# Kernel optimization log

Measured on AMD Instinct MI355X. Metric: run time of the kernel, lower is better.

Reference implementation:

```python
import jax, jax.numpy as jnp
import numpy as np

H, D = 8, 8            # heads, per-head dim (hid_dim = 64)
HID = H * D
L = 6                  # HGTConv layers
NI, NV = 32768, 131072 # num 'instr' / 'var' nodes (batch_size == NI)
E_VV, E_VI, E_IV = 1048576, 524288, 524288
INV_SQRT_D = float(1.0 / np.sqrt(D))


def _seg_softmax(logits, seg, n):
    # softmax over edges grouped by destination node (PyG softmax semantics)
    m = jax.ops.segment_max(logits, seg, num_segments=n)
    m = jnp.where(jnp.isfinite(m), m, 0.0)
    e = jnp.exp(logits - m[seg])
    s = jax.ops.segment_sum(e, seg, num_segments=n)
    return e / (s[seg] + 1e-16)


def _edge_msg(k_src, v_src, q_dst, arel, mrel, prel, src, dst, n_dst):
    # relation-specific transforms: [N_src,H,D] x [H,D,D] -> [N_src,H,D]
    k_rel = jnp.einsum('nhd,hde->nhe', k_src, arel)
    v_rel = jnp.einsum('nhd,hde->nhe', v_src, mrel)
    alpha = jnp.einsum('ehd,ehd->eh', q_dst[dst], k_rel[src]) * prel * INV_SQRT_D  # [E,H]
    w = _seg_softmax(alpha, dst, n_dst)
    return jax.ops.segment_sum(v_rel[src] * w[:, :, None], dst, num_segments=n_dst)


def _kqv(x, Wk, Wq, Wv, bk, bq, bv, n):
    k = (x @ Wk.T + bk).reshape(n, H, D)
    q = (x @ Wq.T + bq).reshape(n, H, D)
    v = (x @ Wv.T + bv).reshape(n, H, D)
    return k, q, v


def _forward(x_instr, x_var,
             Wk_i, Wq_i, Wv_i, Wa_i, bk_i, bq_i, bv_i, ba_i, skip_i,
             Wk_v, Wq_v, Wv_v, Wa_v, bk_v, bq_v, bv_v, ba_v, skip_v,
             arel_vv, mrel_vv, prel_vv, arel_vi, mrel_vi, prel_vi,
             arel_iv, mrel_iv, prel_iv,
             Wqkv, bqkv, Wo, bo,
             mw0, mb0, mw1, mb1, mw2, mb2, mw3, mb3, mw4, mb4, mw5, mb5,
             src_vv, dst_vv, src_vi, dst_vi, src_iv, dst_iv):
    xi, xv = x_instr, x_var
    outs = []
    for l in range(L):
        k_i, q_i, v_i = _kqv(xi, Wk_i[l], Wq_i[l], Wv_i[l], bk_i[l], bq_i[l], bv_i[l], NI)
        k_v, q_v, v_v = _kqv(xv, Wk_v[l], Wq_v[l], Wv_v[l], bk_v[l], bq_v[l], bv_v[l], NV)
        # per-edge-type attention softmax + scatter-sum, then sum over edge types (group='sum')
        agg_v = (_edge_msg(k_v, v_v, q_v, arel_vv[l], mrel_vv[l], prel_vv[l], src_vv, dst_vv, NV)
                 + _edge_msg(k_i, v_i, q_v, arel_iv[l], mrel_iv[l], prel_iv[l], src_iv, dst_iv, NV))
        agg_i = _edge_msg(k_v, v_v, q_i, arel_vi[l], mrel_vi[l], prel_vi[l], src_vi, dst_vi, NI)
        o_i = jax.nn.gelu(agg_i.reshape(NI, HID), approximate=False) @ Wa_i[l].T + ba_i[l]
        b_i = jax.nn.sigmoid(skip_i[l])
        xi = b_i * o_i + (1.0 - b_i) * xi
        o_v = jax.nn.gelu(agg_v.reshape(NV, HID), approximate=False) @ Wa_v[l].T + ba_v[l]
        b_v = jax.nn.sigmoid(skip_v[l])
        xv = b_v * o_v + (1.0 - b_v) * xv
        if l > 0:
            outs.append(xi)
    # jumping-knowledge MultiheadAttention over the L-1 stacked layer outputs
    x = jnp.stack(outs)                        # [S, NI, HID], S = L-1 = 5
    S = x.shape[0]
    qkv = x @ Wqkv.T + bqkv                    # [S, NI, 3*HID]
    q, k, v = jnp.split(qkv, 3, axis=-1)
    q = q.reshape(S, NI, H, D)
    k = k.reshape(S, NI, H, D)
    v = v.reshape(S, NI, H, D)
    sc = jnp.einsum('snhd,tnhd->nhst', q, k) * INV_SQRT_D
    w = jax.nn.softmax(sc, axis=-1)
    o = jnp.einsum('nhst,tnhd->snhd', w, v).reshape(S, NI, HID)
    o = o @ Wo.T + bo
    out = o.sum(axis=0)                        # [NI, HID]; batch_size == NI so view is identity
    for W, b in ((mw0, mb0), (mw1, mb1), (mw2, mb2), (mw3, mb3), (mw4, mb4)):
        out = jax.nn.gelu(out @ W.T + b, approximate=False)
    out = out @ mw5.T + mb5                    # [NI, 1]
    return out[:, 0]


def setup_inputs() -> dict:
    key = jax.random.key(0)
    ks = iter(jax.random.split(key, 64))
    def nrm(shape, scale=1.0):
        return jax.random.normal(next(ks), shape, dtype=jnp.float32) * scale
    d = {}
    d['x_instr'] = nrm((NI, HID))
    d['x_var'] = nrm((NV, HID))
    for t in ('i', 'v'):
        for p in ('Wk', 'Wq', 'Wv', 'Wa'):
            d[f'{p}_{t}'] = nrm((L, HID, HID), (2.0 / HID) ** 0.5)
        for p in ('bk', 'bq', 'bv', 'ba'):
            d[f'{p}_{t}'] = jnp.zeros((L, HID), jnp.float32)
        d[f'skip_{t}'] = jnp.ones((L,), jnp.float32)
    for e in ('vv', 'vi', 'iv'):
        d[f'arel_{e}'] = nrm((L, H, D, D), (1.0 / D) ** 0.5)
        d[f'mrel_{e}'] = nrm((L, H, D, D), (1.0 / D) ** 0.5)
        d[f'prel_{e}'] = jnp.ones((L, H), jnp.float32)
    d['Wqkv'] = nrm((3 * HID, HID), (2.0 / HID) ** 0.5)
    d['bqkv'] = jnp.zeros((3 * HID,), jnp.float32)
    d['Wo'] = nrm((HID, HID), (2.0 / HID) ** 0.5)
    d['bo'] = jnp.zeros((HID,), jnp.float32)
    dims = [64, 32, 16, 8, 4, 2, 1]
    for i in range(6):
        d[f'mw{i}'] = nrm((dims[i + 1], dims[i]), (2.0 / dims[i]) ** 0.5)
        d[f'mb{i}'] = jnp.zeros((dims[i + 1],), jnp.float32)
    d['src_vv'] = jax.random.randint(next(ks), (E_VV,), 0, NV, dtype=jnp.int32).astype(jnp.int64)
    d['dst_vv'] = jax.random.randint(next(ks), (E_VV,), 0, NV, dtype=jnp.int32).astype(jnp.int64)
    d['src_vi'] = jax.random.randint(next(ks), (E_VI,), 0, NV, dtype=jnp.int32).astype(jnp.int64)
    d['dst_vi'] = jax.random.randint(next(ks), (E_VI,), 0, NI, dtype=jnp.int32).astype(jnp.int64)
    d['src_iv'] = jax.random.randint(next(ks), (E_IV,), 0, NI, dtype=jnp.int32).astype(jnp.int64)
    d['dst_iv'] = jax.random.randint(next(ks), (E_IV,), 0, NV, dtype=jnp.int32).astype(jnp.int64)
    return d


def reference(x_instr, x_var,
              Wk_i, Wq_i, Wv_i, Wa_i, bk_i, bq_i, bv_i, ba_i, skip_i,
              Wk_v, Wq_v, Wv_v, Wa_v, bk_v, bq_v, bv_v, ba_v, skip_v,
              arel_vv, mrel_vv, prel_vv, arel_vi, mrel_vi, prel_vi,
              arel_iv, mrel_iv, prel_iv,
              Wqkv, bqkv, Wo, bo,
              mw0, mb0, mw1, mb1, mw2, mb2, mw3, mb3, mw4, mb4, mw5, mb5,
              src_vv, dst_vv, src_vi, dst_vi, src_iv, dst_iv):
    return _forward(x_instr, x_var,
                    Wk_i, Wq_i, Wv_i, Wa_i, bk_i, bq_i, bv_i, ba_i, skip_i,
                    Wk_v, Wq_v, Wv_v, Wa_v, bk_v, bq_v, bv_v, ba_v, skip_v,
                    arel_vv, mrel_vv, prel_vv, arel_vi, mrel_vi, prel_vi,
                    arel_iv, mrel_iv, prel_iv,
                    Wqkv, bqkv, Wo, bo,
                    mw0, mb0, mw1, mb1, mw2, mb2, mw3, mb3, mw4, mb4, mw5, mb5,
                    src_vv, dst_vv, src_vi, dst_vi, src_iv, dst_iv)
```

## Files before the change

### kernel.cpp

```cpp
#include <hip/hip_runtime.h>
#include <cmath>

typedef _Float16 f16_t;
typedef __attribute__((ext_vector_type(8))) short short8;
typedef __attribute__((ext_vector_type(8))) _Float16 half8;
typedef __attribute__((ext_vector_type(4))) float f32x4;
typedef _Float16 h2v __attribute__((ext_vector_type(2)));
typedef _Float16 h8 __attribute__((ext_vector_type(8)));

#define NI_N 32768
#define NV_N 131072
#define E_VV 1048576
#define E_VI 524288
#define E_IV 524288
#define NT_N (NV_N+NV_N+NI_N)
#define ET_N (E_VV+E_IV+E_VI)
#define SC_WIN 4
#define LOG2E 1.4426950408889634f
#define CHV 192
#define CHI 64
#define CHQ 256

__device__ __forceinline__ float gelu_f(float x){ return 0.5f*x*(1.0f+erff(x*0.7071067811865476f)); }

__device__ __forceinline__ void splitf16(float v, short& hi, short& lo){
  f16_t h=(f16_t)v;
  hi=__builtin_bit_cast(short,h);
  f16_t l=(f16_t)(v-(float)h);
  lo=__builtin_bit_cast(short,l);
}
__device__ __forceinline__ f32x4 mfma16(short8 a, short8 b, f32x4 c){
  return __builtin_amdgcn_mfma_f32_16x16x32_f16(__builtin_bit_cast(half8,a),__builtin_bit_cast(half8,b),c,0,0,0);
}
__device__ __forceinline__ float fexp2(float x){
#if __has_builtin(__builtin_amdgcn_exp2f)
  return __builtin_amdgcn_exp2f(x);
#else
  return exp2f(x);
#endif
}
__device__ __forceinline__ float ldval(const float* p){ return *p; }
__device__ __forceinline__ float ldval(const f16_t* p){ return (float)*p; }
__device__ __forceinline__ void stval(float* p,float v){ *p=v; }
__device__ __forceinline__ void stval(f16_t* p,float v){ *p=(f16_t)v; }
__device__ __forceinline__ h2v shxor(h2v a,int m){
  return __builtin_bit_cast(h2v,__shfl_xor(__builtin_bit_cast(int,a),m));
}

__global__ __launch_bounds__(256) void k_hist3(const int* __restrict__ dvv,const int* __restrict__ div_,
    const int* __restrict__ dvi,int* __restrict__ cnt){
  int i=blockIdx.x*256+threadIdx.x;
  if(i<E_VV) atomicAdd(&cnt[dvv[i]],1);
  else if(i<E_VV+E_IV) atomicAdd(&cnt[NV_N+div_[i-E_VV]],1);
  else atomicAdd(&cnt[2*NV_N+dvi[i-E_VV-E_IV]],1);
}
__global__ __launch_bounds__(512) void k_scan1(const int* __restrict__ cnt,int N,int* __restrict__ rp,int* __restrict__ bsum){
  __shared__ int sh[512];
  int i=blockIdx.x*512+threadIdx.x;
  int v=(i<N)?cnt[i]:0;
  sh[threadIdx.x]=v; __syncthreads();
  for(int off=1;off<512;off<<=1){
    int t=(threadIdx.x>=(unsigned)off)?sh[threadIdx.x-off]:0; __syncthreads();
    sh[threadIdx.x]+=t; __syncthreads();
  }
  if(i<N) rp[i]=sh[threadIdx.x]-v;
  if(threadIdx.x==511) bsum[blockIdx.x]=sh[511];
}
__global__ __launch_bounds__(1024) void k_scan2(const int* __restrict__ bsum,int* __restrict__ boff,int nb){
  __shared__ int sh[1024];
  int t=threadIdx.x;
  int v=(t<nb)?bsum[t]:0;
  sh[t]=v; __syncthreads();
  for(int off=1;off<1024;off<<=1){
    int x=(t>=(unsigned)off)?sh[t-off]:0; __syncthreads();
    sh[t]+=x; __syncthreads();
  }
  if(t<nb) boff[t]=sh[t]-v;
  if(t==1023) boff[nb]=sh[1023];
}
__global__ __launch_bounds__(512) void k_scan3(int* __restrict__ rp,const int* __restrict__ boff,int* __restrict__ cur,int N,int nb){
  int i=blockIdx.x*512+threadIdx.x;
  if(i<N){ int v=rp[i]+boff[i>>9]; rp[i]=v; cur[i]=v; }
  if(i==0) rp[N]=boff[nb];
}
__global__ __launch_bounds__(256) void k_scatter3w(const int* __restrict__ svv,const int* __restrict__ dvv,
    const int* __restrict__ siv,const int* __restrict__ div_,
    const int* __restrict__ svi,const int* __restrict__ dvi,
    int* __restrict__ cur,int* __restrict__ esrc,int dlo,int dhi){
  int i=blockIdx.x*256+threadIdx.x;
  int d,s;
  if(i<E_VV){ d=dvv[i]; if(d<dlo||d>=dhi) return; s=svv[i]*320; }
  else if(i<E_VV+E_IV){ int j=i-E_VV; d=NV_N+div_[j]; if(d<dlo||d>=dhi) return; s=siv[j]*192; }
  else { int j=i-E_VV-E_IV; d=2*NV_N+dvi[j]; if(d<dlo||d>=dhi) return; s=svi[j]*320; }
  int p=atomicAdd(&cur[d],1); esrc[p]=s;
}

__global__ __launch_bounds__(256) void k_castx(const float* __restrict__ xi_in,const float* __restrict__ xv_in,
    f16_t* __restrict__ xi,f16_t* __restrict__ xv){
  int i=blockIdx.x*256+threadIdx.x;
  if(i<NI_N*64) xi[i]=(f16_t)xi_in[i];
  else { int j=i-NI_N*64; xv[j]=(f16_t)xv_in[j]; }
}

struct FoldArgs{
  const float *Wk_i,*Wq_i,*Wv_i,*bk_i,*bq_i,*bv_i;
  const float *Wk_v,*Wq_v,*Wv_v,*bk_v,*bq_v,*bv_v;
  const float *arel_vv,*mrel_vv,*prel_vv,*arel_vi,*mrel_vi,*prel_vi,*arel_iv,*mrel_iv,*prel_iv;
  const float *Wa_i,*Wa_v;
  short *fwh_var,*fwl_var,*fwh_ins,*fwl_ins,*wah_i,*wal_i,*wah_v,*wal_v;
  float *fwb_var,*fwb_ins;
};
__global__ __launch_bounds__(256) void k_fold6(FoldArgs fa){
  int gid=blockIdx.x*256+threadIdx.x;
  if(gid>=6*640*64) return;
  int l=gid/(640*64);
  int rem=gid-l*640*64;
  int r=rem>>6, c=rem&63;
  if(r>=512){
    int ro=r&63;
    const float* W=(r<576)?fa.Wa_i:fa.Wa_v;
    short *sh=((r<576)?fa.wah_i:fa.wah_v)+l*4096, *sl=((r<576)?fa.wal_i:fa.wal_v)+l*4096;
    short h,lo; splitf16(W[l*4096+ro*64+c],h,lo);
    sh[ro*64+c]=h; sl[ro*64+c]=lo;
    return;
  }
  const float *W,*B,*rel=nullptr,*prl=nullptr;
  short *sh,*sl; float *fwb; int orow,d; bool isq=false;
  if(r<320){
    sh=fa.fwh_var+l*320*64; sl=fa.fwl_var+l*320*64; fwb=fa.fwb_var+l*320;
    d=r&63;
    if(r<64){ W=fa.Wq_v; B=fa.bq_v; orow=d; isq=true; }
    else if(r<128){ W=fa.Wk_v; B=fa.bk_v; rel=fa.arel_vv; prl=fa.prel_vv; orow=64+2*d; }
    else if(r<192){ W=fa.Wv_v; B=fa.bv_v; rel=fa.mrel_vv; orow=64+2*d+1; }
    else if(r<256){ W=fa.Wk_v; B=fa.bk_v; rel=fa.arel_vi; prl=fa.prel_vi; orow=192+2*d; }
    else         { W=fa.Wv_v; B=fa.bv_v; rel=fa.mrel_vi; orow=192+2*d+1; }
  }else{
    int rr=r-320; sh=fa.fwh_ins+l*192*64; sl=fa.fwl_ins+l*192*64; fwb=fa.fwb_ins+l*192;
    d=rr&63;
    if(rr<64){ W=fa.Wq_i; B=fa.bq_i; orow=d; isq=true; }
    else if(rr<128){ W=fa.Wk_i; B=fa.bk_i; rel=fa.arel_iv; prl=fa.prel_iv; orow=64+2*d; }
    else           { W=fa.Wv_i; B=fa.bv_i; rel=fa.mrel_iv; orow=64+2*d+1; }
  }
  float val,bval;
  if(!rel){
    val=W[l*4096+d*64+c]; bval=B[l*64+d];
  }else{
    int h=d>>3, e=d&7;
    float s=prl?prl[l*8+h]*0.3535533905932738f:1.0f;
    float acc=0.f,bacc=0.f;
    #pragma unroll
    for(int dd=0;dd<8;dd++){
      float rv=rel[l*512+h*64+dd*8+e];
      acc += W[l*4096+(h*8+dd)*64+c]*rv;
      bacc+= B[l*64+h*8+dd]*rv;
    }
    val=acc*s; bval=bacc*s;
  }
  if(isq){ val*=LOG2E; bval*=LOG2E; }
  short h2q,lo2; splitf16(val,h2q,lo2);
  sh[orow*64+c]=h2q; sl[orow*64+c]=lo2;
  if(c==0) fwb[orow]=bval;
}

__global__ __launch_bounds__(256) void k_split2(const float* __restrict__ W,int n,short* __restrict__ hi,short* __restrict__ lo){
  int i=blockIdx.x*256+threadIdx.x;
  if(i<n){ short h,l2; splitf16(W[i],h,l2); hi[i]=h; lo[i]=l2; }
}

__device__ __forceinline__ void colres_body(const f16_t* __restrict__ A,int nrb,
    const short* __restrict__ Bh,const short* __restrict__ Bl,
    const float* __restrict__ bias,f16_t* __restrict__ out,int octot,int ocol0,
    int c,int CH,int wave,int lane,int m,int quad,f16_t (*rep)[72])
{
  short8 bhi[4][2], blo[4][2]; float bb[4];
  #pragma unroll
  for(int ot=0;ot<4;ot++){
    size_t o=(size_t)(ocol0+ot*16+m)*64+quad*8;
    bhi[ot][0]=*(const short8*)(Bh+o);    bhi[ot][1]=*(const short8*)(Bh+o+32);
    blo[ot][0]=*(const short8*)(Bl+o);    blo[ot][1]=*(const short8*)(Bl+o+32);
    bb[ot]=bias[ocol0+ot*16+m];
  }
  int rr0=lane>>3, seg=lane&7;
  for(int rb=c;rb<nrb;rb+=CH){
    int row0=rb*64+wave*16;
    const f16_t* ap=A+(size_t)(row0+m)*64+quad*8;
    short8 a0=*(const short8*)(const void*)ap;
    short8 a1=*(const short8*)(const void*)(ap+32);
    f32x4 acc[4];
    #pragma unroll
    for(int ot=0;ot<4;ot++){ f32x4 t={bb[ot],bb[ot],bb[ot],bb[ot]}; acc[ot]=t; }
    #pragma unroll
    for(int ot=0;ot<4;ot++){
      acc[ot]=mfma16(a0,blo[ot][0],acc[ot]);
      acc[ot]=mfma16(a0,bhi[ot][0],acc[ot]);
      acc[ot]=mfma16(a1,blo[ot][1],acc[ot]);
      acc[ot]=mfma16(a1,bhi[ot][1],acc[ot]);
    }
    #pragma unroll
    for(int ot=0;ot<4;ot++)
      #pragma unroll
      for(int r=0;r<4;r++)
        rep[quad*4+r][ot*16+m]=(f16_t)acc[ot][r];
    #pragma unroll
    for(int it=0;it<2;it++){
      int rr=it*8+rr0;
      h8 vals=*(const h8*)&rep[rr][seg*8];
      *(h8*)(out+(size_t)(row0+rr)*octot+ocol0+seg*8)=vals;
    }
  }
}

__global__ __launch_bounds__(256) void k_colres_feat(const f16_t* __restrict__ Av,const f16_t* __restrict__ Ai,
    const short* __restrict__ Bvh,const short* __restrict__ Bvl,const float* __restrict__ biasv,
    const short* __restrict__ Bih,const short* __restrict__ Bil,const float* __restrict__ biasi,
    f16_t* __restrict__ outv,f16_t* __restrict__ outi)
{
  __shared__ f16_t rep[4][16][72];
  const int wave=threadIdx.x>>6, lane=threadIdx.x&63;
  const int m=lane&15, quad=lane>>4;
  int bx=blockIdx.x;
  if(bx<5*CHV){
    int pan=bx/CHV, c=bx%CHV;
    colres_body(Av,NV_N/64,Bvh,Bvl,biasv,outv,320,pan*64,c,CHV,wave,lane,m,quad,rep[wave]);
  }else{
    bx-=5*CHV;
    int pan=bx/CHI, c=bx%CHI;
    colres_body(Ai,NI_N/64,Bih,Bil,biasi,outi,192,pan*64,c,CHI,wave,lane,m,quad,rep[wave]);
  }
}

__global__ __launch_bounds__(256) void k_colres1(const f16_t* __restrict__ A,int nrb,
    const short* __restrict__ Bh,const short* __restrict__ Bl,
    const float* __restrict__ bias,f16_t* __restrict__ out,int octot,int CH)
{
  __shared__ f16_t rep[4][16][72];
  const int wave=threadIdx.x>>6, lane=threadIdx.x&63;
  const int m=lane&15, quad=lane>>4;
  int pan=blockIdx.x/CH, c=blockIdx.x%CH;
  colres_body(A,nrb,Bh,Bl,bias,out,octot,pan*64,c,CH,wave,lane,m,quad,rep[wave]);
}

template<typename AT, typename OT>
__device__ __forceinline__ void gemm_body(const AT* __restrict__ A,int row0,
    const short* __restrict__ Bh,const short* __restrict__ Bl,
    const float* __restrict__ bias,float bias_scale,
    OT* __restrict__ out,int octot,int ocol0,int npanels,int m,int quad,int lane,
    f16_t (*rep)[72])
{
  const AT* ap=A+(size_t)(row0+m)*64+quad*8;
  constexpr bool AF16 = (sizeof(AT)==2);
  short8 ahi[2], alo[2];
  if constexpr(AF16){
    #pragma unroll
    for(int kf=0;kf<2;kf++) ahi[kf]=*(const short8*)(const void*)(ap+kf*32);
  }else{
    #pragma unroll
    for(int kf=0;kf<2;kf++){
      short8 th,tl;
      #pragma unroll
      for(int j=0;j<8;j++){ short h,l2; splitf16(ldval(&ap[kf*32+j]),h,l2); th[j]=h; tl[j]=l2; }
      ahi[kf]=th; alo[kf]=tl;
    }
  }
  for(int pan=0;pan<npanels;pan++){
    int colbase=pan*64;
    short8 bhi[4][2], blo[4][2];
    #pragma unroll
    for(int ot=0;ot<4;ot++){
      size_t o=(size_t)(colbase+ot*16+m)*64+quad*8;
      #pragma unroll
      for(int kf=0;kf<2;kf++){
        bhi[ot][kf]=*(const short8*)(Bh+o+kf*32);
        blo[ot][kf]=*(const short8*)(Bl+o+kf*32);
      }
    }
    f32x4 acc[4];
    #pragma unroll
    for(int ot=0;ot<4;ot++){
      float bv=bias[colbase+ot*16+m]*bias_scale;
      acc[ot][0]=bv; acc[ot][1]=bv; acc[ot][2]=bv; acc[ot][3]=bv;
    }
    #pragma unroll
    for(int ot=0;ot<4;ot++){
      #pragma unroll
      for(int kf=0;kf<2;kf++){
        if constexpr(!AF16) acc[ot]=mfma16(alo[kf],bhi[ot][kf],acc[ot]);
        acc[ot]=mfma16(ahi[kf],blo[ot][kf],acc[ot]);
        acc[ot]=mfma16(ahi[kf],bhi[ot][kf],acc[ot]);
      }
    }
    if constexpr(sizeof(OT)==2){
      #pragma unroll
      for(int ot=0;ot<4;ot++)
        #pragma unroll
        for(int r=0;r<4;r++)
          rep[quad*4+r][ot*16+m]=(f16_t)acc[ot][r];
      #pragma unroll
      for(int it=0;it<2;it++){
        int rr=it*8+(lane>>3), seg=lane&7;
        h8 vals=*(const h8*)&rep[rr][seg*8];
        *(h8*)(out+(size_t)(row0+rr)*octot+ocol0+colbase+seg*8)=vals;
      }
    }else{
      #pragma unroll
      for(int ot=0;ot<4;ot++){
        int col=ocol0+colbase+ot*16+m;
        #pragma unroll
        for(int r=0;r<4;r++){
          int row=row0+quad*4+r;
          stval(&out[(size_t)row*octot+col],acc[ot][r]);
        }
      }
    }
  }
}

template<typename AT, typename OT>
__global__ __launch_bounds__(256) void k_gemm64p(const AT* __restrict__ A,int N,
    const short* __restrict__ Bh,const short* __restrict__ Bl,
    const float* __restrict__ bias,float bias_scale,
    OT* __restrict__ out,int octot,int ocol0,int npanels)
{
  __shared__ f16_t rep[4][16][72];
  const int wave=threadIdx.x>>6, lane=threadIdx.x&63;
  const int m=lane&15, quad=lane>>4;
  const int row0=blockIdx.x*64+wave*16;
  if(row0>=N) return;
  gemm_body<AT,OT>(A,row0,Bh,Bl,bias,bias_scale,out,octot,ocol0,npanels,m,quad,lane,rep[wave]);
}

__global__ __launch_bounds__(256) void k_update2(const f16_t* __restrict__ agg_i,const f16_t* __restrict__ agg_v,
    const short* __restrict__ wah_i,const short* __restrict__ wal_i,
    const short* __restrict__ wah_v,const short* __restrict__ wal_v,
    const float* __restrict__ ba_i,const float* __restrict__ ba_v,
    const float* __restrict__ skip_i,const float* __restrict__ skip_v,
    f16_t* __restrict__ x_i,f16_t* __restrict__ x_v,
    f16_t* __restrict__ outs,int nbi)
{
  __shared__ f16_t rep[4][16][72];
  const int wave=threadIdx.x>>6, lane=threadIdx.x&63;
  const int m=lane&15, quad=lane>>4;
  const bool isI=(int)blockIdx.x<nbi;
  const int row0=(isI?blockIdx.x:(blockIdx.x-nbi))*64+wave*16;
  const f16_t* agg=isI?agg_i:agg_v;
  const short* Wah=isI?wah_i:wah_v;
  const short* Wal=isI?wal_i:wal_v;
  const float* ba=isI?ba_i:ba_v;
  const float* skip=isI?skip_i:skip_v;
  f16_t* x=isI?x_i:x_v;
  f16_t* oo=isI?outs:nullptr;
  f16_t (*R)[72]=rep[wave];
  short8 bhi[4][2], blo[4][2];
  #pragma unroll
  for(int ot=0;ot<4;ot++){
    size_t o=(size_t)(ot*16+m)*64+quad*8;
    #pragma unroll
    for(int kf=0;kf<2;kf++){
      bhi[ot][kf]=*(const short8*)(Wah+o+kf*32);
      blo[ot][kf]=*(const short8*)(Wal+o+kf*32);
    }
  }
  const f16_t* ap=agg+(size_t)(row0+m)*64+quad*8;
  short8 ahi[2], alo[2];
  #pragma unroll
  for(int kf=0;kf<2;kf++){
    short8 th,tl;
    #pragma unroll
    for(int j=0;j<8;j++){ short h,l2; splitf16(gelu_f((float)ap[kf*32+j]),h,l2); th[j]=h; tl[j]=l2; }
    ahi[kf]=th; alo[kf]=tl;
  }
  int rr0=lane>>3, seg=lane&7;
  h8 x0=*(const h8*)(x+(size_t)(row0+rr0)*64+seg*8);
  h8 x1=*(const h8*)(x+(size_t)(row0+8+rr0)*64+seg*8);
  *(h8*)&R[rr0][seg*8]=x0;
  *(h8*)&R[8+rr0][seg*8]=x1;
  f32x4 acc[4];
  #pragma unroll
  for(int ot=0;ot<4;ot++){
    float bv=ba[ot*16+m];
    acc[ot][0]=bv; acc[ot][1]=bv; acc[ot][2]=bv; acc[ot][3]=bv;
  }
  #pragma unroll
  for(int ot=0;ot<4;ot++){
    #pragma unroll
    for(int kf=0;kf<2;kf++){
      acc[ot]=mfma16(alo[kf],bhi[ot][kf],acc[ot]);
      acc[ot]=mfma16(ahi[kf],blo[ot][kf],acc[ot]);
      acc[ot]=mfma16(ahi[kf],bhi[ot][kf],acc[ot]);
    }
  }
  float s=1.0f/(1.0f+__expf(-skip[0]));
  #pragma unroll
  for(int ot=0;ot<4;ot++){
    int col=ot*16+m;
    #pragma unroll
    for(int r=0;r<4;r++){
      int row=quad*4+r;
      float xn=s*acc[ot][r]+(1.0f-s)*(float)R[row][col];
      R[row][col]=(f16_t)xn;
    }
  }
  h8 o0=*(const h8*)&R[rr0][seg*8];
  h8 o1=*(const h8*)&R[8+rr0][seg*8];
  *(h8*)(x+(size_t)(row0+rr0)*64+seg*8)=o0;
  *(h8*)(x+(size_t)(row0+8+rr0)*64+seg*8)=o1;
  if(oo){
    *(h8*)(oo+(size_t)(row0+rr0)*64+seg*8)=o0;
    *(h8*)(oo+(size_t)(row0+8+rr0)*64+seg*8)=o1;
  }
}

__device__ __forceinline__ float edge_agg8(const int* __restrict__ rp,const int* __restrict__ es,
    const f16_t* __restrict__ sf,int koff,int n,int lane,f16_t qh)
{
  int b=__builtin_amdgcn_readfirstlane(rp[n]);
  int e=__builtin_amdgcn_readfirstlane(rp[n+1]);
  if(b==e) return 0.f;
  float m=-INFINITY, ls=0.f, acc=0.f;
  h2v q2={qh,qh};
  const int lo2=koff+2*lane;
  for(int i=b;i<e;i+=8){
    int o[8];
    #pragma unroll
    for(int j=0;j<8;j++){
      int idx=i+j; idx=(idx<e)?idx:(e-1);
      o[j]=__builtin_amdgcn_readfirstlane(es[idx]);
    }
    h2v kv[8];
    #pragma unroll
    for(int j=0;j<8;j++) kv[j]=*(const h2v*)(sf+(size_t)(unsigned)o[j]+lo2);
    float p[8];
    #pragma unroll
    for(int jp=0;jp<4;jp++){
      h2v pa={kv[2*jp][0],kv[2*jp+1][0]};
      pa=q2*pa;
      pa=pa+shxor(pa,1);
      pa=pa+shxor(pa,2);
      pa=pa+shxor(pa,4);
      p[2*jp]=(float)pa[0]; p[2*jp+1]=(float)pa[1];
    }
    #pragma unroll
    for(int j=0;j<8;j++) p[j]=(i+j<e)?p[j]:-INFINITY;
    float t0=fmaxf(p[0],p[1]),t1=fmaxf(p[2],p[3]),t2=fmaxf(p[4],p[5]),t3=fmaxf(p[6],p[7]);
    float mn=fmaxf(fmaxf(fmaxf(t0,t1),fmaxf(t2,t3)),m);
    float sc=fexp2(m-mn);
    float w[8];
    #pragma unroll
    for(int j=0;j<8;j++) w[j]=fexp2(p[j]-mn);
    float sw=((w[0]+w[1])+(w[2]+w[3]))+((w[4]+w[5])+(w[6]+w[7]));
    float sa=w[0]*(float)kv[0][1]; sa=fmaf(w[1],(float)kv[1][1],sa);
    float sb=w[2]*(float)kv[2][1]; sb=fmaf(w[3],(float)kv[3][1],sb);
    float sg=w[4]*(float)kv[4][1]; sg=fmaf(w[5],(float)kv[5][1],sg);
    float sd=w[6]*(float)kv[6][1]; sd=fmaf(w[7],(float)kv[7][1],sd);
    ls=fmaf(ls,sc,sw);
    acc=fmaf(acc,sc,(sa+sb)+(sg+sd));
    m=mn;
  }
  return acc/(ls+1e-16f);
}

__global__ __launch_bounds__(256) void k_edge_all(const int* __restrict__ rp_all,const int* __restrict__ es,
    const f16_t* __restrict__ var_feat,const f16_t* __restrict__ ins_feat,
    f16_t* __restrict__ agg_v,f16_t* __restrict__ agg_i,int nbv)
{
  int wave=threadIdx.x>>6, lane=threadIdx.x&63;
  if((int)blockIdx.x<nbv){
    int n=blockIdx.x*4+wave;
    f16_t qh=var_feat[(size_t)n*320+lane];
    float r1=edge_agg8(rp_all,es,var_feat,64,n,lane,qh);
    float r2=edge_agg8(rp_all+NV_N,es,ins_feat,64,n,lane,qh);
    agg_v[(size_t)n*64+lane]=(f16_t)(r1+r2);
  }else{
    int n=(blockIdx.x-nbv)*4+wave;
    f16_t qh=ins_feat[(size_t)n*192+lane];
    float r=edge_agg8(rp_all+2*NV_N,es,var_feat,192,n,lane,qh);
    agg_i[(size_t)n*64+lane]=(f16_t)r;
  }
}

__global__ __launch_bounds__(256) void k_jk(const f16_t* __restrict__ qkv,float* __restrict__ osum,int n_nodes){
  int wave=threadIdx.x>>6, lane=threadIdx.x&63;
  int n=blockIdx.x*4+wave;
  if(n>=n_nodes) return;
  float q[5],k[5],v[5];
  #pragma unroll
  for(int s=0;s<5;s++){
    const f16_t* p=qkv+((size_t)s*n_nodes+n)*192;
    q[s]=(float)p[lane]; k[s]=(float)p[64+lane]; v[s]=(float)p[128+lane];
  }
  float sc[5][5];
  #pragma unroll
  for(int s=0;s<5;s++)
    #pragma unroll
    for(int t=0;t<5;t++){
      float x=q[s]*k[t];
      x+=__shfl_xor(x,1); x+=__shfl_xor(x,2); x+=__shfl_xor(x,4);
      sc[s][t]=x*0.3535533905932738f;
    }
  float os=0.f;
  #pragma unroll
  for(int s=0;s<5;s++){
    float m=sc[s][0];
    #pragma unroll
    for(int t=1;t<5;t++) m=fmaxf(m,sc[s][t]);
    float den=0.f, acc=0.f;
    #pragma unroll
    for(int t=0;t<5;t++){ float e=__expf(sc[s][t]-m); den+=e; acc+=e*v[t]; }
    os+=acc/den;
  }
  osum[(size_t)n*64+lane]=os;
}

struct MlpArgs{ const float *w0,*b0,*w1,*b1,*w2,*b2,*w3,*b3,*w4,*b4,*w5,*b5; };
__global__ __launch_bounds__(256) void k_mlp(const float* __restrict__ in,MlpArgs ma,float* __restrict__ out,int N){
  __shared__ float sw0[2048],sb0[32],sw1[512],sb1[16],sw2[128],sb2[8],sw3[32],sb3[4],sw4[8],sb4[2],sw5[2],sb5[1];
  for(int i=threadIdx.x;i<2048;i+=256) sw0[i]=ma.w0[i];
  for(int i=threadIdx.x;i<512;i+=256)  sw1[i]=ma.w1[i];
  if(threadIdx.x<128) sw2[threadIdx.x]=ma.w2[threadIdx.x];
  if(threadIdx.x<32){ sb0[threadIdx.x]=ma.b0[threadIdx.x]; sw3[threadIdx.x]=ma.w3[threadIdx.x]; }
  if(threadIdx.x<16) sb1[threadIdx.x]=ma.b1[threadIdx.x];
  if(threadIdx.x<8){ sb2[threadIdx.x]=ma.b2[threadIdx.x]; sw4[threadIdx.x]=ma.w4[threadIdx.x]; }
  if(threadIdx.x<4) sb3[threadIdx.x]=ma.b3[threadIdx.x];
  if(threadIdx.x<2){ sb4[threadIdx.x]=ma.b4[threadIdx.x]; sw5[threadIdx.x]=ma.w5[threadIdx.x]; }
  if(threadIdx.x==0) sb5[0]=ma.b5[0];
  __syncthreads();
  int n=blockIdx.x*256+threadIdx.x;
  if(n>=N) return;
  float a[64];
  const f32x4* p4=(const f32x4*)(in+(size_t)n*64);
  #pragma unroll
  for(int j=0;j<16;j++){ f32x4 t=p4[j]; a[4*j]=t[0]; a[4*j+1]=t[1]; a[4*j+2]=t[2]; a[4*j+3]=t[3]; }
  float h1[32];
  #pragma unroll
  for(int o=0;o<32;o++){ float s=sb0[o];
    #pragma unroll
    for(int c=0;c<64;c++) s+=a[c]*sw0[o*64+c];
    h1[o]=gelu_f(s); }
  float h2q[16];
  #pragma unroll
  for(int o=0;o<16;o++){ float s=sb1[o];
    #pragma unroll
    for(int c=0;c<32;c++) s+=h1[c]*sw1[o*32+c];
    h2q[o]=gelu_f(s); }
  float h3[8];
  #pragma unroll
  for(int o=0;o<8;o++){ float s=sb2[o];
    #pragma unroll
    for(int c=0;c<16;c++) s+=h2q[c]*sw2[o*16+c];
    h3[o]=gelu_f(s); }
  float h4[4];
  #pragma unroll
  for(int o=0;o<4;o++){ float s=sb3[o];
    #pragma unroll
    for(int c=0;c<8;c++) s+=h3[c]*sw3[o*8+c];
    h4[o]=gelu_f(s); }
  float h5[2];
  #pragma unroll
  for(int o=0;o<2;o++){ float s=sb4[o];
    #pragma unroll
    for(int c=0;c<4;c++) s+=h4[c]*sw4[o*4+c];
    h5[o]=gelu_f(s); }
  float r=sb5[0]+h5[0]*sw5[0]+h5[1]*sw5[1];
  out[n]=r;
}

extern "C" void kernel_launch(void* const* d_in,const int* in_sizes,int n_in,
                              void* d_out,int out_size,void* d_ws,size_t ws_size,
                              hipStream_t stream){
  (void)in_sizes;(void)n_in;(void)out_size;(void)ws_size;
  const float* x_instr=(const float*)d_in[0];
  const float* x_var  =(const float*)d_in[1];
  const float* ba_i=(const float*)d_in[9];
  const float* skip_i=(const float*)d_in[10];
  const float* ba_v=(const float*)d_in[18];
  const float* skip_v=(const float*)d_in[19];
  const float* Wqkv=(const float*)d_in[29];
  const float* bqkv=(const float*)d_in[30];
  const float* Wo=(const float*)d_in[31];
  const float* bo=(const float*)d_in[32];
  const int* src_vv=(const int*)d_in[45];
  const int* dst_vv=(const int*)d_in[46];
  const int* src_vi=(const int*)d_in[47];
  const int* dst_vi=(const int*)d_in[48];
  const int* src_iv=(const int*)d_in[49];
  const int* dst_iv=(const int*)d_in[50];

  char* w=(char*)d_ws;
  auto alloc=[&](size_t b)->char*{ char* p=w; w+=(b+255)&~(size_t)255; return p; };
  int* rp_all=(int*)alloc((size_t)(NT_N+1)*4);
  int* cnt_all=(int*)alloc((size_t)NT_N*4);
  int* cur_all=(int*)alloc((size_t)NT_N*4);
  int* bsum =(int*)alloc(640*4);
  int* boff =(int*)alloc(640*4);
  int* esrc_all=(int*)alloc((size_t)ET_N*4);
  short* fwh_var=(short*)alloc((size_t)6*320*64*2);
  short* fwl_var=(short*)alloc((size_t)6*320*64*2);
  float* fwb_var=(float*)alloc((size_t)6*320*4);
  short* fwh_ins=(short*)alloc((size_t)6*192*64*2);
  short* fwl_ins=(short*)alloc((size_t)6*192*64*2);
  float* fwb_ins=(float*)alloc((size_t)6*192*4);
  short* wah_i=(short*)alloc((size_t)6*64*64*2);
  short* wal_i=(short*)alloc((size_t)6*64*64*2);
  short* wah_v=(short*)alloc((size_t)6*64*64*2);
  short* wal_v=(short*)alloc((size_t)6*64*64*2);
  short* qkvh=(short*)alloc(192*64*2);
  short* qkvl=(short*)alloc(192*64*2);
  short* woh=(short*)alloc(64*64*2);
  short* wol=(short*)alloc(64*64*2);
  f16_t* outs=(f16_t*)alloc((size_t)5*NI_N*64*2);
  char* arena=alloc((size_t)146800640);
  f16_t*  xv      =(f16_t*)(arena);
  f16_t*  xi      =(f16_t*)(arena+16777216);
  f16_t*  var_feat=(f16_t*)(arena+20971520);
  f16_t*  ins_feat=(f16_t*)(arena+104857600);
  f16_t*  agg_v   =(f16_t*)(arena+117440512);
  f16_t*  agg_i   =(f16_t*)(arena+134217728);
  f16_t*  qkv    =(f16_t*)(arena);
  float*  osum   =(float*)(arena+67108864);
  float*  out_jk =(float*)(arena+75497472);

  hipMemsetAsync(cnt_all,0,(size_t)NT_N*4,stream);
  k_hist3<<<ET_N/256,256,0,stream>>>(dst_vv,dst_iv,dst_vi,cnt_all);
  int nb=NT_N/512;
  k_scan1<<<nb,512,0,stream>>>(cnt_all,NT_N,rp_all,bsum);
  k_scan2<<<1,1024,0,stream>>>(bsum,boff,nb);
  k_scan3<<<nb,512,0,stream>>>(rp_all,boff,cur_all,NT_N,nb);
  for(int wdx=0;wdx<SC_WIN;wdx++){
    int dlo=wdx*(NT_N/SC_WIN), dhi=(wdx+1)*(NT_N/SC_WIN);
    k_scatter3w<<<ET_N/256,256,0,stream>>>(src_vv,dst_vv,src_iv,dst_iv,src_vi,dst_vi,cur_all,esrc_all,dlo,dhi);
  }

  k_castx<<<(NI_N*64+NV_N*64)/256,256,0,stream>>>(x_instr,x_var,xi,xv);

  k_split2<<<(192*64+255)/256,256,0,stream>>>(Wqkv,192*64,qkvh,qkvl);
  k_split2<<<(64*64+255)/256,256,0,stream>>>(Wo,64*64,woh,wol);

  FoldArgs fa;
  fa.Wk_i=(const float*)d_in[2]; fa.Wq_i=(const float*)d_in[3]; fa.Wv_i=(const float*)d_in[4];
  fa.bk_i=(const float*)d_in[6]; fa.bq_i=(const float*)d_in[7]; fa.bv_i=(const float*)d_in[8];
  fa.Wk_v=(const float*)d_in[11]; fa.Wq_v=(const float*)d_in[12]; fa.Wv_v=(const float*)d_in[13];
  fa.bk_v=(const float*)d_in[15]; fa.bq_v=(const float*)d_in[16]; fa.bv_v=(const float*)d_in[17];
  fa.arel_vv=(const float*)d_in[20]; fa.mrel_vv=(const float*)d_in[21]; fa.prel_vv=(const float*)d_in[22];
  fa.arel_vi=(const float*)d_in[23]; fa.mrel_vi=(const float*)d_in[24]; fa.prel_vi=(const float*)d_in[25];
  fa.arel_iv=(const float*)d_in[26]; fa.mrel_iv=(const float*)d_in[27]; fa.prel_iv=(const float*)d_in[28];
  fa.Wa_i=(const float*)d_in[5]; fa.Wa_v=(const float*)d_in[14];
  fa.fwh_var=fwh_var; fa.fwl_var=fwl_var; fa.fwh_ins=fwh_ins; fa.fwl_ins=fwl_ins;
  fa.wah_i=wah_i; fa.wal_i=wal_i; fa.wah_v=wah_v; fa.wal_v=wal_v;
  fa.fwb_var=fwb_var; fa.fwb_ins=fwb_ins;
  k_fold6<<<(6*640*64)/256,256,0,stream>>>(fa);

  for(int l=0;l<6;l++){
    k_colres_feat<<<5*CHV+3*CHI,256,0,stream>>>(xv,xi,
        fwh_var+(size_t)l*320*64,fwl_var+(size_t)l*320*64,fwb_var+l*320,
        fwh_ins+(size_t)l*192*64,fwl_ins+(size_t)l*192*64,fwb_ins+l*192,
        var_feat,ins_feat);
    k_edge_all<<<NV_N/4+NI_N/4,256,0,stream>>>(rp_all,esrc_all,var_feat,ins_feat,agg_v,agg_i,NV_N/4);
    k_update2<<<NI_N/64+NV_N/64,256,0,stream>>>(agg_i,agg_v,
        wah_i+(size_t)l*4096,wal_i+(size_t)l*4096,wah_v+(size_t)l*4096,wal_v+(size_t)l*4096,
        ba_i+l*64,ba_v+l*64,skip_i+l,skip_v+l,xi,xv,
        (l>0)?(outs+(size_t)(l-1)*NI_N*64):nullptr,NI_N/64);
  }

  k_colres1<<<3*CHQ,256,0,stream>>>(outs,5*NI_N/64,qkvh,qkvl,bqkv,qkv,192,CHQ);
  k_jk<<<NI_N/4,256,0,stream>>>(qkv,osum,NI_N);
  k_gemm64p<float,float><<<NI_N/64,256,0,stream>>>(osum,NI_N,woh,wol,bo,5.0f,out_jk,64,0,1);
  MlpArgs ma;
  ma.w0=(const float*)d_in[33]; ma.b0=(const float*)d_in[34];
  ma.w1=(const float*)d_in[35]; ma.b1=(const float*)d_in[36];
  ma.w2=(const float*)d_in[37]; ma.b2=(const float*)d_in[38];
  ma.w3=(const float*)d_in[39]; ma.b3=(const float*)d_in[40];
  ma.w4=(const float*)d_in[41]; ma.b4=(const float*)d_in[42];
  ma.w5=(const float*)d_in[43]; ma.b5=(const float*)d_in[44];
  k_mlp<<<NI_N/256,256,0,stream>>>(out_jk,ma,(float*)d_out,NI_N);
}
```

Baseline: 1.636 ms.

## Remap edge aggregation lanes to edge-slot×head with contiguous K/V layout

The folded projection output now stores K and V rows as separate contiguous blocks instead of interleaving them per dimension. The edge aggregation kernel assigns each lane one edge slot and one head, loads 8-wide K and V vectors, and computes the logit with fdot2. This replaces the per-dimension xor-shuffle reductions. Per-slot online-softmax partials are combined across slots with shuffles and an LDS reduction, which adds shared memory use and an end-of-node reduction in exchange for fewer shuffles and wider gathers.

```diff
diff --git a/kernel.cpp b/kernel.cpp
--- a/kernel.cpp
+++ b/kernel.cpp
@@ -7,6 +7,7 @@
 typedef __attribute__((ext_vector_type(4))) float f32x4;
 typedef _Float16 h2v __attribute__((ext_vector_type(2)));
 typedef _Float16 h8 __attribute__((ext_vector_type(8)));
+typedef float f2 __attribute__((ext_vector_type(2)));
 
 #define NI_N 32768
 #define NV_N 131072
@@ -43,9 +44,6 @@
 __device__ __forceinline__ float ldval(const f16_t* p){ return (float)*p; }
 __device__ __forceinline__ void stval(float* p,float v){ *p=v; }
 __device__ __forceinline__ void stval(f16_t* p,float v){ *p=(f16_t)v; }
-__device__ __forceinline__ h2v shxor(h2v a,int m){
-  return __builtin_bit_cast(h2v,__shfl_xor(__builtin_bit_cast(int,a),m));
-}
 
 __global__ __launch_bounds__(256) void k_hist3(const int* __restrict__ dvv,const int* __restrict__ div_,
     const int* __restrict__ dvi,int* __restrict__ cnt){
@@ -125,22 +123,21 @@
     return;
   }
   const float *W,*B,*rel=nullptr,*prl=nullptr;
-  short *sh,*sl; float *fwb; int orow,d; bool isq=false;
+  short *sh,*sl; float *fwb; int orow; bool isq=false;
   if(r<320){
-    sh=fa.fwh_var+l*320*64; sl=fa.fwl_var+l*320*64; fwb=fa.fwb_var+l*320;
-    d=r&63;
-    if(r<64){ W=fa.Wq_v; B=fa.bq_v; orow=d; isq=true; }
-    else if(r<128){ W=fa.Wk_v; B=fa.bk_v; rel=fa.arel_vv; prl=fa.prel_vv; orow=64+2*d; }
-    else if(r<192){ W=fa.Wv_v; B=fa.bv_v; rel=fa.mrel_vv; orow=64+2*d+1; }
-    else if(r<256){ W=fa.Wk_v; B=fa.bk_v; rel=fa.arel_vi; prl=fa.prel_vi; orow=192+2*d; }
-    else         { W=fa.Wv_v; B=fa.bv_v; rel=fa.mrel_vi; orow=192+2*d+1; }
+    sh=fa.fwh_var+l*320*64; sl=fa.fwl_var+l*320*64; fwb=fa.fwb_var+l*320; orow=r;
+    if(r<64){ W=fa.Wq_v; B=fa.bq_v; isq=true; }
+    else if(r<128){ W=fa.Wk_v; B=fa.bk_v; rel=fa.arel_vv; prl=fa.prel_vv; }
+    else if(r<192){ W=fa.Wv_v; B=fa.bv_v; rel=fa.mrel_vv; }
+    else if(r<256){ W=fa.Wk_v; B=fa.bk_v; rel=fa.arel_vi; prl=fa.prel_vi; }
+    else         { W=fa.Wv_v; B=fa.bv_v; rel=fa.mrel_vi; }
   }else{
-    int rr=r-320; sh=fa.fwh_ins+l*192*64; sl=fa.fwl_ins+l*192*64; fwb=fa.fwb_ins+l*192;
-    d=rr&63;
-    if(rr<64){ W=fa.Wq_i; B=fa.bq_i; orow=d; isq=true; }
-    else if(rr<128){ W=fa.Wk_i; B=fa.bk_i; rel=fa.arel_iv; prl=fa.prel_iv; orow=64+2*d; }
-    else           { W=fa.Wv_i; B=fa.bv_i; rel=fa.mrel_iv; orow=64+2*d+1; }
-  }
+    int rr=r-320; sh=fa.fwh_ins+l*192*64; sl=fa.fwl_ins+l*192*64; fwb=fa.fwb_ins+l*192; orow=rr;
+    if(rr<64){ W=fa.Wq_i; B=fa.bq_i; isq=true; }
+    else if(rr<128){ W=fa.Wk_i; B=fa.bk_i; rel=fa.arel_iv; prl=fa.prel_iv; }
+    else           { W=fa.Wv_i; B=fa.bv_i; rel=fa.mrel_iv; }
+  }
+  int d=orow&63;
   float val,bval;
   if(!rel){
     val=W[l*4096+d*64+c]; bval=B[l*64+d];
@@ -410,70 +407,93 @@
   }
 }
 
-__device__ __forceinline__ float edge_agg8(const int* __restrict__ rp,const int* __restrict__ es,
-    const f16_t* __restrict__ sf,int koff,int n,int lane,f16_t qh)
+__device__ __forceinline__ float edge_agg_eh(const int* __restrict__ rp,const int* __restrict__ es,
+    const f16_t* __restrict__ sf,int koff,int voff,int n,int e_slot,int h,int lane,
+    h2v q0,h2v q1,h2v q2,h2v q3,float* __restrict__ L)
 {
   int b=__builtin_amdgcn_readfirstlane(rp[n]);
   int e=__builtin_amdgcn_readfirstlane(rp[n+1]);
   if(b==e) return 0.f;
-  float m=-INFINITY, ls=0.f, acc=0.f;
-  h2v q2={qh,qh};
-  const int lo2=koff+2*lane;
+  const float M0=-1e30f;
+  float m=M0, ls=0.f;
+  f2 A0={0.f,0.f},A1={0.f,0.f},A2={0.f,0.f},A3={0.f,0.f};
+  const int hb=h*8;
   for(int i=b;i<e;i+=8){
-    int o[8];
-    #pragma unroll
-    for(int j=0;j<8;j++){
-      int idx=i+j; idx=(idx<e)?idx:(e-1);
-      o[j]=__builtin_amdgcn_readfirstlane(es[idx]);
-    }
-    h2v kv[8];
-    #pragma unroll
-    for(int j=0;j<8;j++) kv[j]=*(const h2v*)(sf+(size_t)(unsigned)o[j]+lo2);
-    float p[8];
-    #pragma unroll
-    for(int jp=0;jp<4;jp++){
-      h2v pa={kv[2*jp][0],kv[2*jp+1][0]};
-      pa=q2*pa;
-      pa=pa+shxor(pa,1);
-      pa=pa+shxor(pa,2);
-      pa=pa+shxor(pa,4);
-      p[2*jp]=(float)pa[0]; p[2*jp+1]=(float)pa[1];
-    }
-    #pragma unroll
-    for(int j=0;j<8;j++) p[j]=(i+j<e)?p[j]:-INFINITY;
-    float t0=fmaxf(p[0],p[1]),t1=fmaxf(p[2],p[3]),t2=fmaxf(p[4],p[5]),t3=fmaxf(p[6],p[7]);
-    float mn=fmaxf(fmaxf(fmaxf(t0,t1),fmaxf(t2,t3)),m);
+    int eidx=i+e_slot;
+    bool valid=eidx<e;
+    int ec=valid?eidx:(e-1);
+    int off=es[ec];
+    const f16_t* kp=sf+(size_t)(unsigned)off+koff+hb;
+    h8 kv=*(const h8*)kp;
+    h8 vv=*(const h8*)(sf+(size_t)(unsigned)off+voff+hb);
+    float p;
+#if __has_builtin(__builtin_amdgcn_fdot2)
+    p=__builtin_amdgcn_fdot2((h2v){kv[0],kv[1]},q0,0.f,false);
+    p=__builtin_amdgcn_fdot2((h2v){kv[2],kv[3]},q1,p,false);
+    p=__builtin_amdgcn_fdot2((h2v){kv[4],kv[5]},q2,p,false);
+    p=__builtin_amdgcn_fdot2((h2v){kv[6],kv[7]},q3,p,false);
+#else
+    p=(float)kv[0]*(float)q0[0]+(float)kv[1]*(float)q0[1]
+     +(float)kv[2]*(float)q1[0]+(float)kv[3]*(float)q1[1]
+     +(float)kv[4]*(float)q2[0]+(float)kv[5]*(float)q2[1]
+     +(float)kv[6]*(float)q3[0]+(float)kv[7]*(float)q3[1];
+#endif
+    p=valid?p:M0;
+    float mn=fmaxf(m,p);
     float sc=fexp2(m-mn);
-    float w[8];
-    #pragma unroll
-    for(int j=0;j<8;j++) w[j]=fexp2(p[j]-mn);
-    float sw=((w[0]+w[1])+(w[2]+w[3]))+((w[4]+w[5])+(w[6]+w[7]));
-    float sa=w[0]*(float)kv[0][1]; sa=fmaf(w[1],(float)kv[1][1],sa);
-    float sb=w[2]*(float)kv[2][1]; sb=fmaf(w[3],(float)kv[3][1],sb);
-    float sg=w[4]*(float)kv[4][1]; sg=fmaf(w[5],(float)kv[5][1],sg);
-    float sd=w[6]*(float)kv[6][1]; sd=fmaf(w[7],(float)kv[7][1],sd);
-    ls=fmaf(ls,sc,sw);
-    acc=fmaf(acc,sc,(sa+sb)+(sg+sd));
+    float w=valid?fexp2(p-mn):0.f;
+    ls=fmaf(ls,sc,w);
+    f2 S={sc,sc}, W={w,w};
+    f2 V0={(float)vv[0],(float)vv[1]}, V1={(float)vv[2],(float)vv[3]};
+    f2 V2={(float)vv[4],(float)vv[5]}, V3={(float)vv[6],(float)vv[7]};
+    A0=A0*S+W*V0; A1=A1*S+W*V1; A2=A2*S+W*V2; A3=A3*S+W*V3;
     m=mn;
   }
-  return acc/(ls+1e-16f);
+  float mall=fmaxf(m,__shfl_xor(m,8));
+  mall=fmaxf(mall,__shfl_xor(mall,16));
+  mall=fmaxf(mall,__shfl_xor(mall,32));
+  float scl=fexp2(m-mall);
+  ls*=scl;
+  float lsall=ls+__shfl_xor(ls,8);
+  lsall+=__shfl_xor(lsall,16);
+  lsall+=__shfl_xor(lsall,32);
+  f2 S2={scl,scl};
+  A0*=S2; A1*=S2; A2*=S2; A3*=S2;
+  float* wp=L+e_slot*64+hb;
+  f32x4 w0={A0[0],A0[1],A1[0],A1[1]};
+  f32x4 w1={A2[0],A2[1],A3[0],A3[1]};
+  *(f32x4*)wp=w0;
+  *(f32x4*)(wp+4)=w1;
+  __asm__ volatile("s_waitcnt lgkmcnt(0)" ::: "memory");
+  float r=0.f;
+  #pragma unroll
+  for(int ee=0;ee<8;ee++) r+=L[ee*64+lane];
+  float lsr=__shfl(lsall,lane>>3);
+  return r/(lsr+1e-16f);
 }
 
 __global__ __launch_bounds__(256) void k_edge_all(const int* __restrict__ rp_all,const int* __restrict__ es,
     const f16_t* __restrict__ var_feat,const f16_t* __restrict__ ins_feat,
     f16_t* __restrict__ agg_v,f16_t* __restrict__ agg_i,int nbv)
 {
+  __shared__ float lds[4][512];
   int wave=threadIdx.x>>6, lane=threadIdx.x&63;
+  int e_slot=lane>>3, h=lane&7;
+  float* L=lds[wave];
   if((int)blockIdx.x<nbv){
     int n=blockIdx.x*4+wave;
-    f16_t qh=var_feat[(size_t)n*320+lane];
-    float r1=edge_agg8(rp_all,es,var_feat,64,n,lane,qh);
-    float r2=edge_agg8(rp_all+NV_N,es,ins_feat,64,n,lane,qh);
+    const f16_t* qp=var_feat+(size_t)n*320+h*8;
+    h8 qv=*(const h8*)qp;
+    h2v q0={qv[0],qv[1]},q1={qv[2],qv[3]},q2={qv[4],qv[5]},q3={qv[6],qv[7]};
+    float r1=edge_agg_eh(rp_all,es,var_feat,64,128,n,e_slot,h,lane,q0,q1,q2,q3,L);
+    float r2=edge_agg_eh(rp_all+NV_N,es,ins_feat,64,128,n,e_slot,h,lane,q0,q1,q2,q3,L);
     agg_v[(size_t)n*64+lane]=(f16_t)(r1+r2);
   }else{
     int n=(blockIdx.x-nbv)*4+wave;
-    f16_t qh=ins_feat[(size_t)n*192+lane];
-    float r=edge_agg8(rp_all+2*NV_N,es,var_feat,192,n,lane,qh);
+    const f16_t* qp=ins_feat+(size_t)n*192+h*8;
+    h8 qv=*(const h8*)qp;
+    h2v q0={qv[0],qv[1]},q1={qv[2],qv[3]},q2={qv[4],qv[5]},q3={qv[6],qv[7]};
+    float r=edge_agg_eh(rp_all+2*NV_N,es,var_feat,192,256,n,e_slot,h,lane,q0,q1,q2,q3,L);
     agg_i[(size_t)n*64+lane]=(f16_t)r;
   }
 }
```

New measurement: 1.529 ms. 1.07x faster.
